# Kernel tuning notes

Hardware: AMD Instinct MI355X
Metric: run time of the kernel (lower is better)

Reference implementation:

```python
import jax, jax.numpy as jnp
import numpy as np

# ---- fixed hyperparameters from init_kwargs / module defaults ----
ALPHA = 5.0      # SLAYER surrogate sharpness
C = 0.4          # SLAYER surrogate scale
THR = 1.0
ADAPT_COEFF = 1.0
DT = 1.0
B, T, IN, OUT = 64, 1000, 512, 512


def setup_inputs() -> dict:
    key = jax.random.key(0)
    k = jax.random.split(key, 6)
    x = jax.random.normal(k[0], (B, T, IN), dtype=jnp.float32)
    lim = 1.0 / np.sqrt(IN)
    weight = jax.random.uniform(k[1], (OUT, IN), jnp.float32, -lim, lim)
    bias = jnp.zeros((OUT,), jnp.float32)
    # orthogonal recurrent init (gain 1.0)
    recurrent, _ = jnp.linalg.qr(jax.random.normal(k[2], (OUT, OUT), jnp.float32))
    beta = jax.random.uniform(k[3], (OUT,), jnp.float32, 0.0, 1.0)
    beta2 = jax.random.uniform(k[4], (OUT,), jnp.float32, 0.0, 2.0)
    # fixed tau trainers: decay = exp(-dt / tau)
    decay_v = jnp.full((OUT,), np.exp(-DT / 20.0), jnp.float32)          # tau_soma = 20
    tau_adapt = jax.random.uniform(k[5], (OUT,), jnp.float32, 20.0, 200.0)
    decay_b = jnp.exp(-DT / tau_adapt)
    return {"input_tensor": x, "weight": weight, "bias": bias,
            "recurrent": recurrent, "beta": beta, "beta2": beta2,
            "decay_v": decay_v, "decay_b": decay_b}


def _spike(v_thr):
    # forward value: heaviside(v_thr, 1.0); gradient: SLAYER surrogate
    sg = jax.lax.stop_gradient
    heavi = sg(jnp.where(v_thr >= 0, 1.0, 0.0).astype(v_thr.dtype))
    surr = sg(C * ALPHA / (2.0 * jnp.exp(jnp.abs(v_thr) * ALPHA)))
    return heavi + (v_thr - sg(v_thr)) * surr


def _alif_forward(input_tensor, weight, bias, recurrent, beta, beta2, decay_v, decay_b):
    b_sz = input_tensor.shape[0]
    out_f = weight.shape[0]
    z0 = jnp.zeros((b_sz, out_f), input_tensor.dtype)
    # precompute feedforward soma currents for all timesteps: [T, B, OUT]
    cur_in = jnp.einsum('bti,oi->tbo', input_tensor, weight) + bias

    def step(carry, c_t):
        v, z, b = carry
        v = v * (1.0 - z)                          # reset to zero on spike
        cur = c_t + z @ recurrent.T                # recurrent current
        v_t = decay_v * v + (1.0 - decay_v) * (cur - b)
        z_t = _spike(v_t - THR)
        b_t = decay_b * b + (1.0 - decay_b) * (beta * v_t + beta2 * z_t) * ADAPT_COEFF
        return (v_t, z_t, b_t), (v_t, z_t, b_t)

    _, (vs, zs, bs) = jax.lax.scan(step, (z0, z0, z0), cur_in)
    # [T,B,O] -> [B,T,O]
    vs, zs, bs = (jnp.swapaxes(a, 0, 1) for a in (vs, zs, bs))
    pad = z0[:, None, :]                            # initial state at t=0
    v_full = jnp.concatenate([pad, vs], axis=1)
    z_full = jnp.concatenate([pad, zs], axis=1)
    b_full = jnp.concatenate([pad, bs], axis=1)
    states = jnp.stack([v_full, z_full, b_full], axis=0)  # [3, B, T+1, O]
    return zs, states


def reference(input_tensor, weight, bias, recurrent, beta, beta2, decay_v, decay_b):
    return _alif_forward(input_tensor, weight, bias, recurrent, beta, beta2, decay_v, decay_b)
```

## Files before the change

kernel.cpp:

```cpp
#include <hip/hip_runtime.h>
#include <stdint.h>

#define GB   64
#define GT   1000
#define GIN  512
#define GOUT 512
#define GM   (GB*GT)
#define NCH  20
#define CHL  50

typedef __attribute__((ext_vector_type(8))) __bf16 bf8_t;
typedef __attribute__((ext_vector_type(4))) float f4_t;
typedef __attribute__((ext_vector_type(8))) unsigned short us8_t;
typedef __attribute__((ext_vector_type(2))) float f2v;
typedef __attribute__((ext_vector_type(4))) float f4v;

typedef __attribute__((address_space(1))) const uint32_t gu32_t;
typedef __attribute__((address_space(3))) uint32_t lu32_t;

static __device__ __forceinline__ unsigned short f2bf(float f) {
    union { float f; unsigned u; } v; v.f = f;
    unsigned r = v.u + 0x7fffu + ((v.u >> 16) & 1u);
    return (unsigned short)(r >> 16);
}

static __device__ __forceinline__ unsigned short f2h(float f) {
    _Float16 h = (_Float16)f;
    unsigned short s; __builtin_memcpy(&s, &h, 2);
    return s;
}
static __device__ __forceinline__ float lo_h(uint32_t u) {
    unsigned short s = (unsigned short)(u & 0xffffu);
    _Float16 h; __builtin_memcpy(&h, &s, 2);
    return (float)h;
}
static __device__ __forceinline__ float hi_h(uint32_t u) {
    unsigned short s = (unsigned short)(u >> 16);
    _Float16 h; __builtin_memcpy(&h, &s, 2);
    return (float)h;
}
static __device__ __forceinline__ void nts2(float* p, float x, float y) {
    f2v v = {x, y};
    __builtin_nontemporal_store(v, (f2v*)p);
}

#define NX8 4096000
#define NW8 32768
__global__ __launch_bounds__(256) void alif_cvt(
    const float* __restrict__ X, const float* __restrict__ W,
    unsigned short* __restrict__ Xh, unsigned short* __restrict__ Wh,
    unsigned int* __restrict__ flag)
{
    if (blockIdx.x == 0 && threadIdx.x == 0) *flag = 0u;
    const size_t i = (size_t)blockIdx.x * 256 + threadIdx.x;
    const float* src; unsigned short* dst;
    if (i < NX8) { src = X + i * 8; dst = Xh + i * 8; }
    else         { const size_t j = i - NX8; src = W + j * 8; dst = Wh + j * 8; }
    const f4v a = __builtin_nontemporal_load((const f4v*)src);
    const f4v b = __builtin_nontemporal_load((const f4v*)src + 1);
    us8_t r;
    r[0] = f2bf(a.x); r[1] = f2bf(a.y); r[2] = f2bf(a.z); r[3] = f2bf(a.w);
    r[4] = f2bf(b.x); r[5] = f2bf(b.y); r[6] = f2bf(b.z); r[7] = f2bf(b.w);
    *(us8_t*)dst = r;
}

template<bool HALF>
__global__ __launch_bounds__(256) void alif_gemm(
    const unsigned short* __restrict__ Xh, const unsigned short* __restrict__ Wh,
    const float* __restrict__ bias, float* __restrict__ cur,
    unsigned short* __restrict__ curh)
{
    __shared__ unsigned short As[128 * 32];
    __shared__ unsigned short Bs[128 * 32];
    const int tid  = threadIdx.x;
    const int bn   = blockIdx.x & 3;
    const int bm   = blockIdx.x >> 2;
    const int lane = tid & 63;
    const int wave = tid >> 6;
    const int wm   = (wave >> 1) * 64;
    const int wn   = (wave & 1) * 64;
    const int quad = lane >> 4;
    const int l15  = lane & 15;
    const int srow = lane >> 2;
    const int scol = (lane & 3) * 8;

    f4_t acc[4][4];
    #pragma unroll
    for (int i = 0; i < 4; ++i)
        #pragma unroll
        for (int j = 0; j < 4; ++j) acc[i][j] = (f4_t)(0.0f);

    for (int k0 = 0; k0 < GIN; k0 += 32) {
        #pragma unroll
        for (int s = wave; s < 8; s += 4) {
            const int row = s * 16 + srow;
            const unsigned short* ga = Xh + (size_t)(bm * 128 + row) * GIN + k0 + scol;
            const unsigned short* gb = Wh + (size_t)(bn * 128 + row) * GIN + k0 + scol;
            __builtin_amdgcn_global_load_lds((gu32_t*)ga, (lu32_t*)&As[s * 512], 16, 0, 0);
            __builtin_amdgcn_global_load_lds((gu32_t*)gb, (lu32_t*)&Bs[s * 512], 16, 0, 0);
        }
        __syncthreads();
        bf8_t afr[4], bfr[4];
        #pragma unroll
        for (int i = 0; i < 4; ++i) {
            afr[i] = *(const bf8_t*)(&As[(wm + i * 16 + l15) * 32 + quad * 8]);
            bfr[i] = *(const bf8_t*)(&Bs[(wn + i * 16 + l15) * 32 + quad * 8]);
        }
        #pragma unroll
        for (int i = 0; i < 4; ++i)
            #pragma unroll
            for (int j = 0; j < 4; ++j)
                acc[i][j] = __builtin_amdgcn_mfma_f32_16x16x32_bf16(afr[i], bfr[j], acc[i][j], 0, 0, 0);
        __syncthreads();
    }

    float bcs[4];
    #pragma unroll
    for (int j = 0; j < 4; ++j) bcs[j] = bias[bn * 128 + wn + j * 16 + l15];
    #pragma unroll
    for (int i = 0; i < 4; ++i) {
        const int rowb = bm * 128 + wm + i * 16 + quad * 4;
        #pragma unroll
        for (int r = 0; r < 4; ++r) {
            #pragma unroll
            for (int j = 0; j < 4; ++j) {
                const int col  = bn * 128 + wn + j * 16 + l15;
                const float v  = acc[i][j][r] + bcs[j];
                if constexpr (HALF)
                    curh[(size_t)(rowb + r) * GOUT + col] = f2h(v);
                else
                    cur[(size_t)(rowb + r) * GOUT + col] = v;
            }
        }
    }
}

static __device__ __forceinline__ void alif_mat(
    float dv, float db, float be,
    float& a00, float& a01, float& a10, float& a11, float& g0, float& g1)
{
    a00 = dv;
    a01 = -(1.0f - dv);
    g0  = (1.0f - dv);
    a10 = (1.0f - db) * be * dv;
    a11 = db - (1.0f - db) * be * (1.0f - dv);
    g1  = (1.0f - db) * be * (1.0f - dv);
}

__global__ __launch_bounds__(256) void alif_pass1_h(
    const unsigned short* __restrict__ curh,
    const float* __restrict__ beta, const float* __restrict__ decay_v,
    const float* __restrict__ decay_b, float2* __restrict__ u)
{
    const int gid = blockIdx.x * 256 + threadIdx.x;
    const int o2  = gid & 255;
    const int o   = o2 * 2;
    const int r   = gid >> 8;
    const int c   = r % NCH;
    const int b   = r / NCH;
    const float2 dv2 = ((const float2*)decay_v)[o2];
    const float2 db2 = ((const float2*)decay_b)[o2];
    const float2 be2 = ((const float2*)beta)[o2];
    float a00, a01, a10, a11, g0, g1;
    float A00, A01, A10, A11, G0, G1;
    alif_mat(dv2.x, db2.x, be2.x, a00, a01, a10, a11, g0, g1);
    alif_mat(dv2.y, db2.y, be2.y, A00, A01, A10, A11, G0, G1);

    const uint32_t* cp = (const uint32_t*)(curh + ((size_t)b * GT + (size_t)c * CHL) * GOUT + o);
    float v0 = 0.f, w0 = 0.f, v1 = 0.f, w1 = 0.f;
    uint32_t buf[10];
    #pragma unroll
    for (int j = 0; j < 10; ++j) buf[j] = cp[(size_t)j * 256];
    for (int t0 = 0; t0 < CHL; t0 += 10) {
        uint32_t nxt[10];
        const bool more = (t0 + 10 < CHL);
        if (more) {
            #pragma unroll
            for (int j = 0; j < 10; ++j) nxt[j] = cp[(size_t)(t0 + 10 + j) * 256];
        }
        #pragma unroll
        for (int j = 0; j < 10; ++j) {
            const float c0 = lo_h(buf[j]);
            const float c1 = hi_h(buf[j]);
            float nv = a00 * v0 + a01 * w0 + g0 * c0;
            float nw = a10 * v0 + a11 * w0 + g1 * c0;
            v0 = nv; w0 = nw;
            nv = A00 * v1 + A01 * w1 + G0 * c1;
            nw = A10 * v1 + A11 * w1 + G1 * c1;
            v1 = nv; w1 = nw;
        }
        if (more) {
            #pragma unroll
            for (int j = 0; j < 10; ++j) buf[j] = nxt[j];
        }
    }
    f4v s = {v0, w0, v1, w1};
    *(f4v*)(u + ((size_t)b * NCH + c) * GOUT + o) = s;
}

__global__ __launch_bounds__(256) void alif_pass1(
    const float* __restrict__ out,
    const float* __restrict__ beta, const float* __restrict__ decay_v,
    const float* __restrict__ decay_b, float2* __restrict__ u)
{
    const int gid = blockIdx.x * 256 + threadIdx.x;
    const int o = gid & (GOUT - 1);
    const int r = gid >> 9;
    const int c = r % NCH;
    const int b = r / NCH;
    float a00, a01, a10, a11, g0, g1;
    alif_mat(decay_v[o], decay_b[o], beta[o], a00, a01, a10, a11, g0, g1);

    const float* cp = out + ((size_t)b * GT + c * CHL) * GOUT + o;
    float v = 0.f, w = 0.f;
    float buf[10];
    #pragma unroll
    for (int j = 0; j < 10; ++j) buf[j] = cp[(size_t)j * GOUT];
    for (int t0 = 0; t0 < CHL; t0 += 10) {
        float nxt[10];
        const bool more = (t0 + 10 < CHL);
        if (more) {
            #pragma unroll
            for (int j = 0; j < 10; ++j) nxt[j] = cp[(size_t)(t0 + 10 + j) * GOUT];
        }
        #pragma unroll
        for (int j = 0; j < 10; ++j) {
            const float cu = buf[j];
            const float nv = a00 * v + a01 * w + g0 * cu;
            const float nw = a10 * v + a11 * w + g1 * cu;
            v = nv; w = nw;
        }
        if (more) {
            #pragma unroll
            for (int j = 0; j < 10; ++j) buf[j] = nxt[j];
        }
    }
    u[((size_t)b * NCH + c) * GOUT + o] = make_float2(v, w);
}

__global__ __launch_bounds__(256) void alif_pass2(
    float2* __restrict__ u,
    const float* __restrict__ beta, const float* __restrict__ decay_v,
    const float* __restrict__ decay_b)
{
    const int gid = blockIdx.x * 256 + threadIdx.x;
    const int o = gid & (GOUT - 1);
    const int b = gid >> 9;
    float a00, a01, a10, a11, g0, g1;
    alif_mat(decay_v[o], decay_b[o], beta[o], a00, a01, a10, a11, g0, g1);
    float p00 = 1.f, p01 = 0.f, p10 = 0.f, p11 = 1.f;
    for (int i = 0; i < CHL; ++i) {
        const float n00 = a00 * p00 + a01 * p10, n01 = a00 * p01 + a01 * p11;
        const float n10 = a10 * p00 + a11 * p10, n11 = a10 * p01 + a11 * p11;
        p00 = n00; p01 = n01; p10 = n10; p11 = n11;
    }
    float Sv = 0.f, Sb = 0.f;
    for (int c = 0; c < NCH; ++c) {
        const size_t idx = ((size_t)b * NCH + c) * GOUT + o;
        const float2 t = u[idx];
        u[idx] = make_float2(Sv, Sb);
        const float nSv = p00 * Sv + p01 * Sb + t.x;
        const float nSb = p10 * Sv + p11 * Sb + t.y;
        Sv = nSv; Sb = nSb;
    }
}

__global__ __launch_bounds__(256) void alif_pass3_h(
    const unsigned short* __restrict__ curh, float* __restrict__ out,
    const float2* __restrict__ seed,
    const float* __restrict__ beta, const float* __restrict__ beta2,
    const float* __restrict__ decay_v, const float* __restrict__ decay_b,
    unsigned int* __restrict__ flag)
{
    const int gid = blockIdx.x * 256 + threadIdx.x;
    const int o2  = gid & 255;
    const int o   = o2 * 2;
    const int r   = gid >> 8;
    const int c   = r % NCH;
    const int b   = r / NCH;
    const float2 dv2 = ((const float2*)decay_v)[o2];
    const float2 db2 = ((const float2*)decay_b)[o2];
    const float2 be_ = ((const float2*)beta)[o2];
    const float2 b2_ = ((const float2*)beta2)[o2];

    const int tbase = c * CHL;
    const uint32_t* cp = (const uint32_t*)(curh + ((size_t)b * GT + tbase) * GOUT + o);
    float* zsp = out + ((size_t)b * GT + tbase) * GOUT + o;
    const size_t SB = (size_t)GB * GT * GOUT;
    const size_t PL = (size_t)GB * (GT + 1) * GOUT;
    float* vf  = out + SB + ((size_t)b * (GT + 1) + tbase + 1) * GOUT + o;
    float* zf  = vf + PL;
    float* bfp = vf + 2 * PL;
    if (c == 0) {
        nts2(vf  - GOUT, 0.f, 0.f);
        nts2(zf  - GOUT, 0.f, 0.f);
        nts2(bfp - GOUT, 0.f, 0.f);
    }

    const f4v s0 = *(const f4v*)(seed + ((size_t)b * NCH + c) * GOUT + o);
    float v0 = s0.x, ba0 = s0.y, v1 = s0.z, ba1 = s0.w;
    float z0 = 0.f, z1 = 0.f;
    bool any = false;
    uint32_t buf[10];
    #pragma unroll
    for (int j = 0; j < 10; ++j) buf[j] = cp[(size_t)j * 256];

    for (int t0 = 0; t0 < CHL; t0 += 10) {
        uint32_t nxt[10];
        const bool more = (t0 + 10 < CHL);
        if (more) {
            #pragma unroll
            for (int j = 0; j < 10; ++j) nxt[j] = cp[(size_t)(t0 + 10 + j) * 256];
        }
        #pragma unroll
        for (int j = 0; j < 10; ++j) {
            const int t = t0 + j;
            const float c0 = lo_h(buf[j]);
            const float c1 = hi_h(buf[j]);
            v0 *= (1.0f - z0);
            v0 = dv2.x * v0 + (1.0f - dv2.x) * (c0 - ba0);
            z0 = (v0 >= 1.0f) ? 1.0f : 0.0f;
            ba0 = db2.x * ba0 + (1.0f - db2.x) * (be_.x * v0 + b2_.x * z0);
            v1 *= (1.0f - z1);
            v1 = dv2.y * v1 + (1.0f - dv2.y) * (c1 - ba1);
            z1 = (v1 >= 1.0f) ? 1.0f : 0.0f;
            ba1 = db2.y * ba1 + (1.0f - db2.y) * (be_.y * v1 + b2_.y * z1);
            any = any || (z0 != 0.0f) || (z1 != 0.0f);
            nts2(zsp + (size_t)t * GOUT, z0, z1);
            nts2(vf  + (size_t)t * GOUT, v0, v1);
            nts2(zf  + (size_t)t * GOUT, z0, z1);
            nts2(bfp + (size_t)t * GOUT, ba0, ba1);
        }
        if (more) {
            #pragma unroll
            for (int j = 0; j < 10; ++j) buf[j] = nxt[j];
        }
    }
    if (any) atomicOr(flag, 1u);
}

__global__ __launch_bounds__(256) void alif_pass3(
    float* __restrict__ out, const float2* __restrict__ seed,
    const float* __restrict__ beta, const float* __restrict__ beta2,
    const float* __restrict__ decay_v, const float* __restrict__ decay_b,
    unsigned int* __restrict__ flag)
{
    const int gid = blockIdx.x * 256 + threadIdx.x;
    const int o = gid & (GOUT - 1);
    const int r = gid >> 9;
    const int c = r % NCH;
    const int b = r / NCH;
    const float dv = decay_v[o], db = decay_b[o];
    const float be = beta[o],    be2 = beta2[o];

    const int tbase = c * CHL;
    float* curp = out + ((size_t)b * GT + tbase) * GOUT + o;
    const size_t SB = (size_t)GB * GT * GOUT;
    const size_t PL = (size_t)GB * (GT + 1) * GOUT;
    float* vf  = out + SB + ((size_t)b * (GT + 1) + tbase + 1) * GOUT + o;
    float* zf  = vf + PL;
    float* bfp = vf + 2 * PL;
    if (c == 0) {
        vf[-(ptrdiff_t)GOUT] = 0.f; zf[-(ptrdiff_t)GOUT] = 0.f; bfp[-(ptrdiff_t)GOUT] = 0.f;
    }

    const float2 s0 = seed[((size_t)b * NCH + c) * GOUT + o];
    float v = s0.x, ba = s0.y, z = 0.f;
    bool any = false;
    float buf[10];
    #pragma unroll
    for (int j = 0; j < 10; ++j) buf[j] = curp[(size_t)j * GOUT];

    for (int t0 = 0; t0 < CHL; t0 += 10) {
        float nxt[10];
        const bool more = (t0 + 10 < CHL);
        if (more) {
            #pragma unroll
            for (int j = 0; j < 10; ++j) nxt[j] = curp[(size_t)(t0 + 10 + j) * GOUT];
        }
        #pragma unroll
        for (int j = 0; j < 10; ++j) {
            const int t = t0 + j;
            v *= (1.0f - z);
            v = dv * v + (1.0f - dv) * (buf[j] - ba);
            z = (v >= 1.0f) ? 1.0f : 0.0f;
            ba = db * ba + (1.0f - db) * (be * v + be2 * z);
            any = any || (z != 0.0f);
            curp[(size_t)t * GOUT]     = z;
            vf[(size_t)t * GOUT]       = v;
            zf[(size_t)t * GOUT]       = z;
            bfp[(size_t)t * GOUT]      = ba;
        }
        if (more) {
            #pragma unroll
            for (int j = 0; j < 10; ++j) buf[j] = nxt[j];
        }
    }
    if (any) atomicOr(flag, 1u);
}

__global__ __launch_bounds__(128) void alif_scan(
    float* __restrict__ out,
    const float* __restrict__ beta, const float* __restrict__ beta2,
    const float* __restrict__ decay_v, const float* __restrict__ decay_b,
    unsigned int* __restrict__ flag)
{
    const int gid = blockIdx.x * 128 + threadIdx.x;
    const int o = gid & (GOUT - 1);
    const int b = gid >> 9;
    const float dv = decay_v[o], db = decay_b[o];
    const float be = beta[o],    be2 = beta2[o];
    float* curp = out + (size_t)b * GT * GOUT + o;
    const size_t SB = (size_t)GB * GT * GOUT;
    const size_t PL = (size_t)GB * (GT + 1) * GOUT;
    float* vf  = out + SB + (size_t)b * (GT + 1) * GOUT + o;
    float* zf  = vf + PL;
    float* bfp = vf + 2 * PL;
    vf[0] = 0.f; zf[0] = 0.f; bfp[0] = 0.f;
    float v = 0.f, z = 0.f, ba = 0.f;
    bool any = false;
    float buf[8];
    #pragma unroll
    for (int j = 0; j < 8; ++j) buf[j] = curp[(size_t)j * GOUT];
    for (int t0 = 0; t0 < GT; t0 += 8) {
        float nxt[8];
        const bool more = (t0 + 8 < GT);
        if (more) {
            #pragma unroll
            for (int j = 0; j < 8; ++j) nxt[j] = curp[(size_t)(t0 + 8 + j) * GOUT];
        }
        #pragma unroll
        for (int j = 0; j < 8; ++j) {
            const int t = t0 + j;
            v *= (1.0f - z);
            v = dv * v + (1.0f - dv) * (buf[j] - ba);
            z = (v >= 1.0f) ? 1.0f : 0.0f;
            ba = db * ba + (1.0f - db) * (be * v + be2 * z);
            any = any || (z != 0.0f);
            curp[(size_t)t * GOUT]      = z;
            vf[(size_t)(t + 1) * GOUT]  = v;
            zf[(size_t)(t + 1) * GOUT]  = z;
            bfp[(size_t)(t + 1) * GOUT] = ba;
        }
        if (more) {
            #pragma unroll
            for (int j = 0; j < 8; ++j) buf[j] = nxt[j];
        }
    }
    if (any) atomicOr(flag, 1u);
}

__global__ __launch_bounds__(512) void alif_exact(
    const float* __restrict__ X, const float* __restrict__ W,
    const float* __restrict__ bias, const float* __restrict__ R,
    const float* __restrict__ beta, const float* __restrict__ beta2,
    const float* __restrict__ decay_v, const float* __restrict__ decay_b,
    float* __restrict__ out, const unsigned int* __restrict__ flag)
{
    if (*flag == 0u) return;
    const int b = blockIdx.x;
    const int o = threadIdx.x;
    __shared__ float xs[GIN];
    __shared__ float zsh[GOUT];
    __shared__ int sflag;
    const float dv = decay_v[o], db = decay_b[o];
    const float be = beta[o],    be2 = beta2[o];
    const float bi = bias[o];
    float* zsp = out + (size_t)b * GT * GOUT + o;
    const size_t SB = (size_t)GB * GT * GOUT, PL = (size_t)GB * (GT + 1) * GOUT;
    float* vf  = out + SB + (size_t)b * (GT + 1) * GOUT + o;
    float* zf  = vf + PL;
    float* bfp = vf + 2 * PL;
    vf[0] = 0.f; zf[0] = 0.f; bfp[0] = 0.f;
    float v = 0.f, z = 0.f, ba = 0.f;
    const float* wr = W + (size_t)o * GIN;
    const float* rr = R + (size_t)o * GOUT;
    for (int t = 0; t < GT; ++t) {
        __syncthreads();
        xs[o]  = X[((size_t)b * GT + t) * GIN + o];
        zsh[o] = z;
        if (o == 0) sflag = 0;
        __syncthreads();
        if (z != 0.f) sflag = 1;
        __syncthreads();
        float cur = bi;
        #pragma unroll 8
        for (int i = 0; i < GIN; ++i) cur += wr[i] * xs[i];
        if (sflag) {
            #pragma unroll 8
            for (int i = 0; i < GOUT; ++i) cur += rr[i] * zsh[i];
        }
        v *= (1.f - z);
        v = dv * v + (1.f - dv) * (cur - ba);
        z = (v >= 1.f) ? 1.f : 0.f;
        ba = db * ba + (1.f - db) * (be * v + be2 * z);
        zsp[(size_t)t * GOUT]       = z;
        vf[(size_t)(t + 1) * GOUT]  = v;
        zf[(size_t)(t + 1) * GOUT]  = z;
        bfp[(size_t)(t + 1) * GOUT] = ba;
    }
}

extern "C" void kernel_launch(void* const* d_in, const int* in_sizes, int n_in,
                              void* d_out, int out_size, void* d_ws, size_t ws_size,
                              hipStream_t stream)
{
    const float* X     = (const float*)d_in[0];
    const float* W     = (const float*)d_in[1];
    const float* bias  = (const float*)d_in[2];
    const float* R     = (const float*)d_in[3];
    const float* beta  = (const float*)d_in[4];
    const float* beta2 = (const float*)d_in[5];
    const float* dv    = (const float*)d_in[6];
    const float* db    = (const float*)d_in[7];
    float* out = (float*)d_out;
    unsigned int* flag = (unsigned int*)d_ws;

    const size_t SB = (size_t)GB * GT * GOUT;
    unsigned short* Xh = (unsigned short*)(out + SB);
    unsigned short* Wh = Xh + (size_t)GM * GIN;

    const size_t seeds_b = (size_t)GB * NCH * GOUT * sizeof(float2);
    const size_t need_f  = 256 + seeds_b;
    const size_t need_h  = need_f + (size_t)GM * GOUT * 2;

    alif_cvt<<<dim3((NX8 + NW8) / 256), dim3(256), 0, stream>>>(X, W, Xh, Wh, flag);

    if (ws_size >= need_h) {
        float2* u = (float2*)((char*)d_ws + 256);
        unsigned short* curh = (unsigned short*)((char*)d_ws + need_f);
        alif_gemm<true><<<dim3(500 * 4), dim3(256), 0, stream>>>(Xh, Wh, bias, nullptr, curh);
        alif_pass1_h<<<dim3(GB * NCH * GOUT / 512), dim3(256), 0, stream>>>(curh, beta, dv, db, u);
        alif_pass2<<<dim3(GB * GOUT / 256), dim3(256), 0, stream>>>(u, beta, dv, db);
        alif_pass3_h<<<dim3(GB * NCH * GOUT / 512), dim3(256), 0, stream>>>(curh, out, u, beta, beta2, dv, db, flag);
    } else if (ws_size >= need_f) {
        float2* u = (float2*)((char*)d_ws + 256);
        alif_gemm<false><<<dim3(500 * 4), dim3(256), 0, stream>>>(Xh, Wh, bias, out, nullptr);
        alif_pass1<<<dim3(GB * NCH * GOUT / 256), dim3(256), 0, stream>>>(out, beta, dv, db, u);
        alif_pass2<<<dim3(GB * GOUT / 256), dim3(256), 0, stream>>>(u, beta, dv, db);
        alif_pass3<<<dim3(GB * NCH * GOUT / 256), dim3(256), 0, stream>>>(out, u, beta, beta2, dv, db, flag);
    } else {
        alif_gemm<false><<<dim3(500 * 4), dim3(256), 0, stream>>>(Xh, Wh, bias, out, nullptr);
        alif_scan<<<dim3(256), dim3(128), 0, stream>>>(out, beta, beta2, dv, db, flag);
    }
    alif_exact<<<dim3(GB), dim3(512), 0, stream>>>(X, W, bias, R, beta, beta2, dv, db, out, flag);
}
```

Before: 688.4 us.

## Fuse X fp32-to-bf16 conversion into GEMM with full-N tiles and double buffering

```diff
diff --git a/kernel.cpp b/kernel.cpp
--- a/kernel.cpp
+++ b/kernel.cpp
@@ -44,20 +44,17 @@
     __builtin_nontemporal_store(v, (f2v*)p);
 }
 
-#define NX8 4096000
 #define NW8 32768
-__global__ __launch_bounds__(256) void alif_cvt(
-    const float* __restrict__ X, const float* __restrict__ W,
-    unsigned short* __restrict__ Xh, unsigned short* __restrict__ Wh,
+__global__ __launch_bounds__(256) void alif_cvt_w(
+    const float* __restrict__ W, unsigned short* __restrict__ Wh,
     unsigned int* __restrict__ flag)
 {
     if (blockIdx.x == 0 && threadIdx.x == 0) *flag = 0u;
     const size_t i = (size_t)blockIdx.x * 256 + threadIdx.x;
-    const float* src; unsigned short* dst;
-    if (i < NX8) { src = X + i * 8; dst = Xh + i * 8; }
-    else         { const size_t j = i - NX8; src = W + j * 8; dst = Wh + j * 8; }
-    const f4v a = __builtin_nontemporal_load((const f4v*)src);
-    const f4v b = __builtin_nontemporal_load((const f4v*)src + 1);
+    const float* src = W + i * 8;
+    unsigned short* dst = Wh + i * 8;
+    const f4v a = *(const f4v*)src;
+    const f4v b = *((const f4v*)src + 1);
     us8_t r;
     r[0] = f2bf(a.x); r[1] = f2bf(a.y); r[2] = f2bf(a.z); r[3] = f2bf(a.w);
     r[4] = f2bf(b.x); r[5] = f2bf(b.y); r[6] = f2bf(b.z); r[7] = f2bf(b.w);
@@ -65,71 +62,100 @@
 }
 
 template<bool HALF>
-__global__ __launch_bounds__(256) void alif_gemm(
-    const unsigned short* __restrict__ Xh, const unsigned short* __restrict__ Wh,
+__global__ __launch_bounds__(512) void alif_gemmf(
+    const float* __restrict__ X, const unsigned short* __restrict__ Wh,
     const float* __restrict__ bias, float* __restrict__ cur,
     unsigned short* __restrict__ curh)
 {
-    __shared__ unsigned short As[128 * 32];
-    __shared__ unsigned short Bs[128 * 32];
+    __shared__ unsigned short As[2][128 * 32];
+    __shared__ unsigned short Bs[2][512 * 32];
     const int tid  = threadIdx.x;
-    const int bn   = blockIdx.x & 3;
-    const int bm   = blockIdx.x >> 2;
+    const int bm   = blockIdx.x;
     const int lane = tid & 63;
     const int wave = tid >> 6;
-    const int wm   = (wave >> 1) * 64;
-    const int wn   = (wave & 1) * 64;
+    const int wm   = (wave >> 2) * 64;
+    const int wn   = (wave & 3) * 128;
     const int quad = lane >> 4;
     const int l15  = lane & 15;
-    const int srow = lane >> 2;
-    const int scol = (lane & 3) * 8;
-
-    f4_t acc[4][4];
+    const int arow = tid >> 2;
+    const int acol = (tid & 3) * 8;
+    const int brow4 = lane >> 2;
+    const int bcol  = (lane & 3) * 8;
+
+    const size_t m0 = (size_t)bm * 128;
+    const float* ap = X + (m0 + arow) * GIN + acol;
+
+    f4_t acc[4][8];
     #pragma unroll
     for (int i = 0; i < 4; ++i)
         #pragma unroll
-        for (int j = 0; j < 4; ++j) acc[i][j] = (f4_t)(0.0f);
-
-    for (int k0 = 0; k0 < GIN; k0 += 32) {
-        #pragma unroll
-        for (int s = wave; s < 8; s += 4) {
-            const int row = s * 16 + srow;
-            const unsigned short* ga = Xh + (size_t)(bm * 128 + row) * GIN + k0 + scol;
-            const unsigned short* gb = Wh + (size_t)(bn * 128 + row) * GIN + k0 + scol;
-            __builtin_amdgcn_global_load_lds((gu32_t*)ga, (lu32_t*)&As[s * 512], 16, 0, 0);
-            __builtin_amdgcn_global_load_lds((gu32_t*)gb, (lu32_t*)&Bs[s * 512], 16, 0, 0);
+        for (int j = 0; j < 8; ++j) acc[i][j] = (f4_t)(0.0f);
+
+    f4v pa0 = __builtin_nontemporal_load((const f4v*)ap);
+    f4v pa1 = __builtin_nontemporal_load((const f4v*)ap + 1);
+    #pragma unroll
+    for (int s = wave; s < 32; s += 8) {
+        const unsigned short* gb = Wh + (size_t)(s * 16 + brow4) * GIN + bcol;
+        __builtin_amdgcn_global_load_lds((gu32_t*)gb, (lu32_t*)&Bs[0][s * 512], 16, 0, 0);
+    }
+    {
+        us8_t r;
+        r[0] = f2bf(pa0.x); r[1] = f2bf(pa0.y); r[2] = f2bf(pa0.z); r[3] = f2bf(pa0.w);
+        r[4] = f2bf(pa1.x); r[5] = f2bf(pa1.y); r[6] = f2bf(pa1.z); r[7] = f2bf(pa1.w);
+        *(us8_t*)&As[0][arow * 32 + acol] = r;
+    }
+    __syncthreads();
+
+    for (int kk = 0; kk < 16; ++kk) {
+        const int cb = kk & 1;
+        const bool pre = (kk + 1 < 16);
+        if (pre) {
+            const float* apn = ap + (kk + 1) * 32;
+            pa0 = __builtin_nontemporal_load((const f4v*)apn);
+            pa1 = __builtin_nontemporal_load((const f4v*)apn + 1);
+            const int k1 = (kk + 1) * 32;
+            #pragma unroll
+            for (int s = wave; s < 32; s += 8) {
+                const unsigned short* gb = Wh + (size_t)(s * 16 + brow4) * GIN + k1 + bcol;
+                __builtin_amdgcn_global_load_lds((gu32_t*)gb, (lu32_t*)&Bs[cb ^ 1][s * 512], 16, 0, 0);
+            }
+        }
+        bf8_t afr[4];
+        #pragma unroll
+        for (int i = 0; i < 4; ++i)
+            afr[i] = *(const bf8_t*)&As[cb][(wm + i * 16 + l15) * 32 + quad * 8];
+        #pragma unroll
+        for (int j = 0; j < 8; ++j) {
+            const bf8_t bfr = *(const bf8_t*)&Bs[cb][(wn + j * 16 + l15) * 32 + quad * 8];
+            #pragma unroll
+            for (int i = 0; i < 4; ++i)
+                acc[i][j] = __builtin_amdgcn_mfma_f32_16x16x32_bf16(afr[i], bfr, acc[i][j], 0, 0, 0);
+        }
+        if (pre) {
+            us8_t r;
+            r[0] = f2bf(pa0.x); r[1] = f2bf(pa0.y); r[2] = f2bf(pa0.z); r[3] = f2bf(pa0.w);
+            r[4] = f2bf(pa1.x); r[5] = f2bf(pa1.y); r[6] = f2bf(pa1.z); r[7] = f2bf(pa1.w);
+            *(us8_t*)&As[cb ^ 1][arow * 32 + acol] = r;
         }
         __syncthreads();
-        bf8_t afr[4], bfr[4];
-        #pragma unroll
-        for (int i = 0; i < 4; ++i) {
-            afr[i] = *(const bf8_t*)(&As[(wm + i * 16 + l15) * 32 + quad * 8]);
-            bfr[i] = *(const bf8_t*)(&Bs[(wn + i * 16 + l15) * 32 + quad * 8]);
-        }
-        #pragma unroll
-        for (int i = 0; i < 4; ++i)
-            #pragma unroll
-            for (int j = 0; j < 4; ++j)
-                acc[i][j] = __builtin_amdgcn_mfma_f32_16x16x32_bf16(afr[i], bfr[j], acc[i][j], 0, 0, 0);
-        __syncthreads();
-    }
-
-    float bcs[4];
-    #pragma unroll
-    for (int j = 0; j < 4; ++j) bcs[j] = bias[bn * 128 + wn + j * 16 + l15];
+    }
+
+    float bcs[8];
+    #pragma unroll
+    for (int j = 0; j < 8; ++j) bcs[j] = bias[wn + j * 16 + l15];
     #pragma unroll
     for (int i = 0; i < 4; ++i) {
-        const int rowb = bm * 128 + wm + i * 16 + quad * 4;
+        const size_t rowb = m0 + wm + i * 16 + quad * 4;
         #pragma unroll
         for (int r = 0; r < 4; ++r) {
             #pragma unroll
-            for (int j = 0; j < 4; ++j) {
-                const int col  = bn * 128 + wn + j * 16 + l15;
-                const float v  = acc[i][j][r] + bcs[j];
+            for (int j = 0; j < 8; ++j) {
+                const int col = wn + j * 16 + l15;
+                const float v = acc[i][j][r] + bcs[j];
                 if constexpr (HALF)
-                    curh[(size_t)(rowb + r) * GOUT + col] = f2h(v);
+                    curh[(rowb + r) * GOUT + col] = f2h(v);
                 else
-                    cur[(size_t)(rowb + r) * GOUT + col] = v;
+                    cur[(rowb + r) * GOUT + col] = v;
             }
         }
     }
@@ -517,30 +543,29 @@
     unsigned int* flag = (unsigned int*)d_ws;
 
     const size_t SB = (size_t)GB * GT * GOUT;
-    unsigned short* Xh = (unsigned short*)(out + SB);
-    unsigned short* Wh = Xh + (size_t)GM * GIN;
+    unsigned short* Wh = (unsigned short*)(out + SB);
 
     const size_t seeds_b = (size_t)GB * NCH * GOUT * sizeof(float2);
     const size_t need_f  = 256 + seeds_b;
     const size_t need_h  = need_f + (size_t)GM * GOUT * 2;
 
-    alif_cvt<<<dim3((NX8 + NW8) / 256), dim3(256), 0, stream>>>(X, W, Xh, Wh, flag);
+    alif_cvt_w<<<dim3(NW8 / 256), dim3(256), 0, stream>>>(W, Wh, flag);
 
     if (ws_size >= need_h) {
         float2* u = (float2*)((char*)d_ws + 256);
         unsigned short* curh = (unsigned short*)((char*)d_ws + need_f);
-        alif_gemm<true><<<dim3(500 * 4), dim3(256), 0, stream>>>(Xh, Wh, bias, nullptr, curh);
+        alif_gemmf<true><<<dim3(500), dim3(512), 0, stream>>>(X, Wh, bias, nullptr, curh);
         alif_pass1_h<<<dim3(GB * NCH * GOUT / 512), dim3(256), 0, stream>>>(curh, beta, dv, db, u);
         alif_pass2<<<dim3(GB * GOUT / 256), dim3(256), 0, stream>>>(u, beta, dv, db);
         alif_pass3_h<<<dim3(GB * NCH * GOUT / 512), dim3(256), 0, stream>>>(curh, out, u, beta, beta2, dv, db, flag);
     } else if (ws_size >= need_f) {
         float2* u = (float2*)((char*)d_ws + 256);
-        alif_gemm<false><<<dim3(500 * 4), dim3(256), 0, stream>>>(Xh, Wh, bias, out, nullptr);
+        alif_gemmf<false><<<dim3(500), dim3(512), 0, stream>>>(X, Wh, bias, out, nullptr);
         alif_pass1<<<dim3(GB * NCH * GOUT / 256), dim3(256), 0, stream>>>(out, beta, dv, db, u);
         alif_pass2<<<dim3(GB * GOUT / 256), dim3(256), 0, stream>>>(u, beta, dv, db);
         alif_pass3<<<dim3(GB * NCH * GOUT / 256), dim3(256), 0, stream>>>(out, u, beta, beta2, dv, db, flag);
     } else {
-        alif_gemm<false><<<dim3(500 * 4), dim3(256), 0, stream>>>(Xh, Wh, bias, out, nullptr);
+        alif_gemmf<false><<<dim3(500), dim3(512), 0, stream>>>(X, Wh, bias, out, nullptr);
         alif_scan<<<dim3(256), dim3(128), 0, stream>>>(out, beta, beta2, dv, db, flag);
     }
     alif_exact<<<dim3(GB), dim3(512), 0, stream>>>(X, W, bias, R, beta, beta2, dv, db, out, flag);
```

After: 679.7 us. About the same (-1.3%).
